# Performance work log

Hardware: AMD Instinct MI355X
Metric: run time of the kernel (lower is better)

The kernel has to match this reference:

```python
import jax, jax.numpy as jnp
import numpy as np

DIM_IN, DIM_K, DIM_V = 128, 64, 128

def setup_inputs() -> dict:
    key = jax.random.key(0)
    k1, k2, k3, k4 = jax.random.split(key, 4)
    x = jax.random.normal(k1, (8, DIM_IN, 4096), dtype=jnp.float32)
    # nn.Linear(dim_in, dim_out) weight has shape [dim_out, dim_in]; y @ W.T
    Wq = jax.random.normal(k2, (DIM_K, DIM_IN), dtype=jnp.float32) / np.sqrt(DIM_IN)
    Wk = jax.random.normal(k3, (DIM_K, DIM_IN), dtype=jnp.float32) / np.sqrt(DIM_IN)
    Wv = jax.random.normal(k4, (DIM_V, DIM_IN), dtype=jnp.float32) / np.sqrt(DIM_IN)
    return {"x": x, "Wq": Wq, "Wk": Wk, "Wv": Wv}

def reference(x, Wq, Wk, Wv):
    # x: [b, dim_in, n] -> y: [b, n, dim_in]
    y = jnp.swapaxes(x, -1, -2)
    q = jnp.einsum('bnd,kd->bnk', y, Wq)  # [b, n, dim_k]
    k = jnp.einsum('bnd,kd->bnk', y, Wk)  # [b, n, dim_k]
    v = jnp.einsum('bnd,vd->bnv', y, Wv)  # [b, n, dim_v]
    scale = 1.0 / np.sqrt(DIM_K).astype(np.float32)
    dist = jnp.einsum('bik,bjk->bij', q, k) * scale  # [b, n, n]
    dist = jax.nn.softmax(dist, axis=-1)
    att = jnp.einsum('bij,bjv->biv', dist, v)  # [b, n, dim_v]
    att = jnp.swapaxes(att, -1, -2)  # [b, dim_v, n]
    return att + x
```

## Files before the change

kernel.cpp:

```cpp
#include <hip/hip_runtime.h>
#include <hip/hip_bf16.h>
#include <stdint.h>

#define NB   8
#define NSEQ 4096
#define DIN  128
#define DK   64
#define DVV  128

typedef __bf16 bf16x8 __attribute__((ext_vector_type(8)));
typedef float f32x4 __attribute__((ext_vector_type(4)));
typedef unsigned int u32x4v __attribute__((ext_vector_type(4)));
typedef unsigned short u16;
typedef unsigned int u32;

__device__ __forceinline__ u32 cvt_pk_bf16(float lo, float hi) {
  u32 r;
  asm("v_cvt_pk_bf16_f32 %0, %1, %2" : "=v"(r) : "v"(lo), "v"(hi));
  return r;
}

#define GLDS16(G, L)                                                          \
  __builtin_amdgcn_global_load_lds(                                           \
      (__attribute__((address_space(1))) void*)(G),                           \
      (__attribute__((address_space(3))) void*)(L), 16, 0, 0)

__global__ __launch_bounds__(256) void proj(
    const float* __restrict__ x, const float* __restrict__ Wq,
    const float* __restrict__ Wk, const float* __restrict__ Wv,
    u16* __restrict__ Qb, u16* __restrict__ Kb, u16* __restrict__ Vtb) {
  __shared__ alignas(16) u16 xs[64 * 128];
  const int tid = threadIdx.x;
  const int w = tid >> 6, l = tid & 63;
  const int lg = l >> 4, li = l & 15;
  const int b = blockIdx.x & 7;
  const int n0 = (blockIdx.x >> 3) << 6;

  {
    const float* xp = x + ((size_t)b * DIN + w * 32) * NSEQ + n0 + l;
    #pragma unroll
    for (int cc = 0; cc < 4; ++cc) {
      const int c = w * 4 + cc;
      u32 pk[4];
      #pragma unroll
      for (int jj = 0; jj < 4; ++jj) {
        const float f0 = xp[(size_t)(cc * 8 + 2 * jj) * NSEQ];
        const float f1 = xp[(size_t)(cc * 8 + 2 * jj + 1) * NSEQ];
        pk[jj] = cvt_pk_bf16(f0, f1);
      }
      *(uint4*)&xs[l * 128 + ((c ^ (l & 15)) * 8)] = *(uint4*)pk;
    }
  }

  const float* W;
  float scale = 1.0f;
  if (w == 0)      { W = Wq; scale = 0.180336880111120429f; }
  else if (w == 1) { W = Wk; }
  else if (w == 2) { W = Wv; }
  else             { W = Wv + 64 * DIN; }

  bf16x8 wf[4][4];
  #pragma unroll
  for (int ct = 0; ct < 4; ++ct) {
    const float* wr = W + (ct * 16 + li) * DIN + lg * 8;
    #pragma unroll
    for (int ks = 0; ks < 4; ++ks) {
      const float4 f0 = *(const float4*)(wr + 32 * ks);
      const float4 f1 = *(const float4*)(wr + 32 * ks + 4);
      u32x4v pk;
      pk[0] = cvt_pk_bf16(f0.x * scale, f0.y * scale);
      pk[1] = cvt_pk_bf16(f0.z * scale, f0.w * scale);
      pk[2] = cvt_pk_bf16(f1.x * scale, f1.y * scale);
      pk[3] = cvt_pk_bf16(f1.z * scale, f1.w * scale);
      wf[ct][ks] = __builtin_bit_cast(bf16x8, pk);
    }
  }

  __syncthreads();

  const f32x4 fz = {0.f, 0.f, 0.f, 0.f};
  #pragma unroll
  for (int nt = 0; nt < 4; ++nt) {
    const int n16 = n0 + nt * 16;
    bf16x8 xf[4];
    #pragma unroll
    for (int ks = 0; ks < 4; ++ks)
      xf[ks] = *(const bf16x8*)&xs[(nt * 16 + li) * 128 + (((lg + 4 * ks) ^ li) * 8)];
    #pragma unroll
    for (int ct = 0; ct < 4; ++ct) {
      f32x4 acc = fz;
      if (w < 2) {
        #pragma unroll
        for (int ks = 0; ks < 4; ++ks)
          acc = __builtin_amdgcn_mfma_f32_16x16x32_bf16(xf[ks], wf[ct][ks], acc, 0, 0, 0);
        u16* ob = (w == 0 ? Qb : Kb) + (size_t)b * NSEQ * DK;
        #pragma unroll
        for (int r = 0; r < 4; ++r)
          ob[(size_t)(n16 + lg * 4 + r) * DK + ct * 16 + li] =
              (u16)cvt_pk_bf16(acc[r], acc[r]);
      } else {
        #pragma unroll
        for (int ks = 0; ks < 4; ++ks)
          acc = __builtin_amdgcn_mfma_f32_16x16x32_bf16(wf[ct][ks], xf[ks], acc, 0, 0, 0);
        const int chb = (w == 3 ? 64 : 0) + ct * 16 + lg * 4;
        #pragma unroll
        for (int r = 0; r < 4; ++r)
          Vtb[((size_t)b * DVV + chb + r) * NSEQ + n16 + li] =
              (u16)cvt_pk_bf16(acc[r], acc[r]);
      }
    }
  }
}

__global__ __launch_bounds__(256, 2) void attn(
    const u16* __restrict__ Qb, const u16* __restrict__ Kb,
    const u16* __restrict__ Vtb, const float* __restrict__ x,
    float* __restrict__ out) {
  __shared__ alignas(16) char lds[69632];
  const int tid = threadIdx.x;
  const int w = tid >> 6, l = tid & 63;
  const int lg = l >> 4, li = l & 15;
  const int b = blockIdx.x & 7;
  const int qbase = (blockIdx.x >> 3) << 6;

  bf16x8 qf[4][2];
  #pragma unroll
  for (int h = 0; h < 4; ++h) {
    const u16* qp = Qb + ((size_t)(b * NSEQ + qbase + h * 16 + li) * DK + lg * 8);
    qf[h][0] = *(const bf16x8*)qp;
    qf[h][1] = *(const bf16x8*)(qp + 32);
  }

  const f32x4 fzero = {0.f, 0.f, 0.f, 0.f};
  f32x4 oacc[4][8];
  #pragma unroll
  for (int h = 0; h < 4; ++h)
    #pragma unroll
    for (int dt = 0; dt < 8; ++dt) oacc[h][dt] = fzero;
  float lrow[4] = {0.f, 0.f, 0.f, 0.f};

  const u16* kbase = Kb + ((size_t)b * NSEQ + 8 * (li >> 2) + (li & 3)) * DK + lg * 8;
  const u16* vsrc = Vtb + ((size_t)b * DVV + (l >> 2)) * NSEQ + (l & 3) * 8;
  char* const mybuf = lds + w * 16384;

  bf16x8 kf[2][2];
#define KLOAD(T) do {                                                         \
    const u16* kp_ = kbase + (size_t)(T) * 32 * DK;                           \
    _Pragma("unroll") for (int jt = 0; jt < 2; ++jt)                          \
      _Pragma("unroll") for (int kc = 0; kc < 2; ++kc)                        \
        kf[jt][kc] = *(const bf16x8*)(kp_ + jt * 4 * DK + kc * 32);           \
  } while (0)
#define STAGEV(T, B) do {                                                     \
    char* vb_ = mybuf + (B) * 8192;                                           \
    _Pragma("unroll") for (int s = 0; s < 8; ++s)                             \
      GLDS16(vsrc + (size_t)s * 16 * NSEQ + (size_t)(T) * 32, vb_ + s * 1024); \
  } while (0)

  const int t0 = w * 32;
  KLOAD(t0);
  STAGEV(t0, 0);

  #pragma unroll 1
  for (int i = 0; i < 32; ++i) {
    const int t = t0 + i;
    const int cur = i & 1;
    if (i < 31) STAGEV(t + 1, cur ^ 1);

    bf16x8 pf[4];
    __builtin_amdgcn_s_setprio(1);
    #pragma unroll
    for (int h = 0; h < 4; ++h) {
      f32x4 a0 = __builtin_amdgcn_mfma_f32_16x16x32_bf16(kf[0][0], qf[h][0], fzero, 0, 0, 0);
      a0 = __builtin_amdgcn_mfma_f32_16x16x32_bf16(kf[0][1], qf[h][1], a0, 0, 0, 0);
      f32x4 a1 = __builtin_amdgcn_mfma_f32_16x16x32_bf16(kf[1][0], qf[h][0], fzero, 0, 0, 0);
      a1 = __builtin_amdgcn_mfma_f32_16x16x32_bf16(kf[1][1], qf[h][1], a1, 0, 0, 0);
      float p0 = __builtin_amdgcn_exp2f(a0[0]);
      float p1 = __builtin_amdgcn_exp2f(a0[1]);
      float p2 = __builtin_amdgcn_exp2f(a0[2]);
      float p3 = __builtin_amdgcn_exp2f(a0[3]);
      float p4 = __builtin_amdgcn_exp2f(a1[0]);
      float p5 = __builtin_amdgcn_exp2f(a1[1]);
      float p6 = __builtin_amdgcn_exp2f(a1[2]);
      float p7 = __builtin_amdgcn_exp2f(a1[3]);
      lrow[h] += ((p0 + p1) + (p2 + p3)) + ((p4 + p5) + (p6 + p7));
      u32x4v pk;
      pk[0] = cvt_pk_bf16(p0, p1);
      pk[1] = cvt_pk_bf16(p2, p3);
      pk[2] = cvt_pk_bf16(p4, p5);
      pk[3] = cvt_pk_bf16(p6, p7);
      pf[h] = __builtin_bit_cast(bf16x8, pk);
    }
    __builtin_amdgcn_s_setprio(0);

    if (i < 31) KLOAD(t + 1);

    asm volatile("s_waitcnt vmcnt(12)" ::: "memory");
    __builtin_amdgcn_sched_barrier(0);

    const char* vb = mybuf + cur * 8192;
    __builtin_amdgcn_s_setprio(1);
    #pragma unroll
    for (int dt = 0; dt < 8; ++dt) {
      const bf16x8 vf = *(const bf16x8*)(vb + dt * 1024 + li * 64 + lg * 16);
      #pragma unroll
      for (int h = 0; h < 4; ++h)
        oacc[h][dt] = __builtin_amdgcn_mfma_f32_16x16x32_bf16(vf, pf[h], oacc[h][dt], 0, 0, 0);
    }
    __builtin_amdgcn_s_setprio(0);
  }

  #pragma unroll
  for (int h = 0; h < 4; ++h) {
    lrow[h] += __shfl_xor(lrow[h], 16, 64);
    lrow[h] += __shfl_xor(lrow[h], 32, 64);
  }
  float* const bufA = (float*)lds;
  float* const bufB = (float*)(lds + 33792);
  float* const stats = (float*)(lds + 67584);
#define DUMP(DST) do {                                                        \
    _Pragma("unroll") for (int h = 0; h < 4; ++h)                             \
      _Pragma("unroll") for (int dt = 0; dt < 8; ++dt)                        \
        _Pragma("unroll") for (int r = 0; r < 4; ++r)                         \
          (DST)[(dt * 16 + lg * 4 + r) * 66 + h * 16 + li] = oacc[h][dt][r];  \
  } while (0)
#define ADDF(SRC) do {                                                        \
    _Pragma("unroll") for (int h = 0; h < 4; ++h)                             \
      _Pragma("unroll") for (int dt = 0; dt < 8; ++dt)                        \
        _Pragma("unroll") for (int r = 0; r < 4; ++r)                         \
          oacc[h][dt][r] += (SRC)[(dt * 16 + lg * 4 + r) * 66 + h * 16 + li]; \
  } while (0)
#define SAVESTATS(WI) do {                                                    \
    if (lg == 0) {                                                            \
      for (int h = 0; h < 4; ++h) stats[(WI) * 64 + h * 16 + li] = lrow[h];   \
    }                                                                         \
  } while (0)
  __syncthreads();
  if (w == 1) { DUMP(bufA); SAVESTATS(1); }
  if (w == 3) { DUMP(bufB); SAVESTATS(3); }
  __syncthreads();
  if (w == 0) ADDF(bufA);
  if (w == 2) {
    ADDF(bufB);
    #pragma unroll
    for (int h = 0; h < 4; ++h) lrow[h] += stats[3 * 64 + h * 16 + li];
  }
  __syncthreads();
  if (w == 2) { DUMP(bufA); SAVESTATS(2); }
  __syncthreads();
  if (w == 0) {
    ADDF(bufA);
    #pragma unroll
    for (int h = 0; h < 4; ++h) {
      const float ls = lrow[h] + stats[1 * 64 + h * 16 + li] + stats[2 * 64 + h * 16 + li];
      const float rl = 1.0f / ls;
      #pragma unroll
      for (int dt = 0; dt < 8; ++dt) {
        #pragma unroll
        for (int r = 0; r < 4; ++r) {
          const int dv = dt * 16 + lg * 4 + r;
          const size_t idx = ((size_t)b * DVV + dv) * NSEQ + qbase + h * 16 + li;
          out[idx] = oacc[h][dt][r] * rl + x[idx];
        }
      }
    }
  }
#undef KLOAD
#undef STAGEV
#undef DUMP
#undef ADDF
#undef SAVESTATS
}

extern "C" void kernel_launch(void* const* d_in, const int* in_sizes, int n_in,
                              void* d_out, int out_size, void* d_ws, size_t ws_size,
                              hipStream_t stream) {
  const float* x  = (const float*)d_in[0];
  const float* Wq = (const float*)d_in[1];
  const float* Wk = (const float*)d_in[2];
  const float* Wv = (const float*)d_in[3];
  float* out = (float*)d_out;

  u16* qws = (u16*)d_ws;
  u16* kws = qws + (size_t)NB * NSEQ * DK;
  u16* vws = kws + (size_t)NB * NSEQ * DK;

  proj<<<512, 256, 0, stream>>>(x, Wq, Wk, Wv, qws, kws, vws);
  attn<<<512, 256, 0, stream>>>(qws, kws, vws, x, out);
}
```

Baseline: 83.35 us.

## Pre-swizzle K and V into fragment-contiguous tiles for coalesced attention loads

The projection kernel now writes K and V in a tiled layout that matches the MFMA fragment order the attention kernel consumes. Each wave's K fragment loads and V global-to-LDS staging become fully contiguous 16-byte-per-lane reads instead of strided row gathers. The LDS read offset for V is remapped to match, and the reduction buffer stride changes from 66 to 67 floats to cut bank conflicts. In exchange, the projection stores become more scattered, and correctness depends on the index math agreeing across both kernels.

New measurement: 77.67 us. 1.07x faster.

```diff
diff --git a/kernel.cpp b/kernel.cpp
--- a/kernel.cpp
+++ b/kernel.cpp
@@ -28,7 +28,7 @@
 __global__ __launch_bounds__(256) void proj(
     const float* __restrict__ x, const float* __restrict__ Wq,
     const float* __restrict__ Wk, const float* __restrict__ Wv,
-    u16* __restrict__ Qb, u16* __restrict__ Kb, u16* __restrict__ Vtb) {
+    u16* __restrict__ Qb, u16* __restrict__ Kf, u16* __restrict__ Vf) {
   __shared__ alignas(16) u16 xs[64 * 128];
   const int tid = threadIdx.x;
   const int w = tid >> 6, l = tid & 63;
@@ -93,28 +93,48 @@
         #pragma unroll
         for (int ks = 0; ks < 4; ++ks)
           acc = __builtin_amdgcn_mfma_f32_16x16x32_bf16(xf[ks], wf[ct][ks], acc, 0, 0, 0);
-        u16* ob = (w == 0 ? Qb : Kb) + (size_t)b * NSEQ * DK;
-        #pragma unroll
-        for (int r = 0; r < 4; ++r)
-          ob[(size_t)(n16 + lg * 4 + r) * DK + ct * 16 + li] =
-              (u16)cvt_pk_bf16(acc[r], acc[r]);
+        if (w == 0) {
+          u16* ob = Qb + (size_t)b * NSEQ * DK;
+          #pragma unroll
+          for (int r = 0; r < 4; ++r)
+            ob[(size_t)(n16 + lg * 4 + r) * DK + ct * 16 + li] =
+                (u16)cvt_pk_bf16(acc[r], acc[r]);
+        } else {
+          #pragma unroll
+          for (int r = 0; r < 4; ++r) {
+            const int n = n16 + lg * 4 + r;
+            const int t = n >> 5, rowin = n & 31;
+            const int jt = (rowin >> 2) & 1;
+            const int lip = 4 * (rowin >> 3) + (rowin & 3);
+            const int kc = ct >> 1;
+            const int lgp = ((ct & 1) * 16 + li) >> 3;
+            Kf[((size_t)(b * 128 + t)) * 2048 + (jt * 2 + kc) * 512 +
+               (lgp * 16 + lip) * 8 + (li & 7)] = (u16)cvt_pk_bf16(acc[r], acc[r]);
+          }
+        }
       } else {
         #pragma unroll
         for (int ks = 0; ks < 4; ++ks)
           acc = __builtin_amdgcn_mfma_f32_16x16x32_bf16(wf[ct][ks], xf[ks], acc, 0, 0, 0);
         const int chb = (w == 3 ? 64 : 0) + ct * 16 + lg * 4;
         #pragma unroll
-        for (int r = 0; r < 4; ++r)
-          Vtb[((size_t)b * DVV + chb + r) * NSEQ + n16 + li] =
+        for (int r = 0; r < 4; ++r) {
+          const int dv = chb + r;
+          const int n = n16 + li;
+          const int t = n >> 5, kv = n & 31;
+          const int s = dv >> 4;
+          const int lp = (dv & 7) | ((kv >> 3) << 3) | (((dv >> 3) & 1) << 5);
+          Vf[((size_t)(b * 128 + t)) * 4096 + s * 512 + lp * 8 + (kv & 7)] =
               (u16)cvt_pk_bf16(acc[r], acc[r]);
+        }
       }
     }
   }
 }
 
 __global__ __launch_bounds__(256, 2) void attn(
-    const u16* __restrict__ Qb, const u16* __restrict__ Kb,
-    const u16* __restrict__ Vtb, const float* __restrict__ x,
+    const u16* __restrict__ Qb, const u16* __restrict__ Kf,
+    const u16* __restrict__ Vf, const float* __restrict__ x,
     float* __restrict__ out) {
   __shared__ alignas(16) char lds[69632];
   const int tid = threadIdx.x;
@@ -139,26 +159,28 @@
     for (int dt = 0; dt < 8; ++dt) oacc[h][dt] = fzero;
   float lrow[4] = {0.f, 0.f, 0.f, 0.f};
 
-  const u16* kbase = Kb + ((size_t)b * NSEQ + 8 * (li >> 2) + (li & 3)) * DK + lg * 8;
-  const u16* vsrc = Vtb + ((size_t)b * DVV + (l >> 2)) * NSEQ + (l & 3) * 8;
+  const u16* kbase = Kf + (size_t)b * 128 * 2048 + l * 8;
+  const u16* vbase = Vf + (size_t)b * 128 * 4096 + l * 8;
   char* const mybuf = lds + w * 16384;
+  const int vq = (((li & 7) | (lg << 3) | ((li >> 3) << 5)) << 4);
 
   bf16x8 kf[2][2];
 #define KLOAD(T) do {                                                         \
-    const u16* kp_ = kbase + (size_t)(T) * 32 * DK;                           \
+    const u16* kp_ = kbase + (size_t)(T) * 2048;                              \
     _Pragma("unroll") for (int jt = 0; jt < 2; ++jt)                          \
       _Pragma("unroll") for (int kc = 0; kc < 2; ++kc)                        \
-        kf[jt][kc] = *(const bf16x8*)(kp_ + jt * 4 * DK + kc * 32);           \
+        kf[jt][kc] = *(const bf16x8*)(kp_ + (jt * 2 + kc) * 512);             \
   } while (0)
 #define STAGEV(T, B) do {                                                     \
     char* vb_ = mybuf + (B) * 8192;                                           \
+    const u16* vp_ = vbase + (size_t)(T) * 4096;                              \
     _Pragma("unroll") for (int s = 0; s < 8; ++s)                             \
-      GLDS16(vsrc + (size_t)s * 16 * NSEQ + (size_t)(T) * 32, vb_ + s * 1024); \
+      GLDS16(vp_ + s * 512, vb_ + s * 1024);                                  \
   } while (0)
 
   const int t0 = w * 32;
+  STAGEV(t0, 0);
   KLOAD(t0);
-  STAGEV(t0, 0);
 
   #pragma unroll 1
   for (int i = 0; i < 32; ++i) {
@@ -201,7 +223,7 @@
     __builtin_amdgcn_s_setprio(1);
     #pragma unroll
     for (int dt = 0; dt < 8; ++dt) {
-      const bf16x8 vf = *(const bf16x8*)(vb + dt * 1024 + li * 64 + lg * 16);
+      const bf16x8 vf = *(const bf16x8*)(vb + dt * 1024 + vq);
       #pragma unroll
       for (int h = 0; h < 4; ++h)
         oacc[h][dt] = __builtin_amdgcn_mfma_f32_16x16x32_bf16(vf, pf[h], oacc[h][dt], 0, 0, 0);
@@ -215,19 +237,19 @@
     lrow[h] += __shfl_xor(lrow[h], 32, 64);
   }
   float* const bufA = (float*)lds;
-  float* const bufB = (float*)(lds + 33792);
-  float* const stats = (float*)(lds + 67584);
+  float* const bufB = (float*)(lds + 34304);
+  float* const stats = (float*)(lds + 68608);
 #define DUMP(DST) do {                                                        \
     _Pragma("unroll") for (int h = 0; h < 4; ++h)                             \
       _Pragma("unroll") for (int dt = 0; dt < 8; ++dt)                        \
         _Pragma("unroll") for (int r = 0; r < 4; ++r)                         \
-          (DST)[(dt * 16 + lg * 4 + r) * 66 + h * 16 + li] = oacc[h][dt][r];  \
+          (DST)[(dt * 16 + lg * 4 + r) * 67 + h * 16 + li] = oacc[h][dt][r];  \
   } while (0)
 #define ADDF(SRC) do {                                                        \
     _Pragma("unroll") for (int h = 0; h < 4; ++h)                             \
       _Pragma("unroll") for (int dt = 0; dt < 8; ++dt)                        \
         _Pragma("unroll") for (int r = 0; r < 4; ++r)                         \
-          oacc[h][dt][r] += (SRC)[(dt * 16 + lg * 4 + r) * 66 + h * 16 + li]; \
+          oacc[h][dt][r] += (SRC)[(dt * 16 + lg * 4 + r) * 67 + h * 16 + li]; \
   } while (0)
 #define SAVESTATS(WI) do {                                                    \
     if (lg == 0) {                                                            \
```
